# Optimization experiments

Measured on AMD Instinct MI355X. Metric: run time of the kernel, lower is better.

## Reference

```python
import jax, jax.numpy as jnp
import numpy as np
from functools import partial

THRESH = 0.5   # similarity_threshold
EPS = 1e-8     # F.cosine_similarity eps


def setup_inputs() -> dict:
    key = jax.random.key(0)
    # uniform positive vectors -> pairwise cosine ~0.75 > threshold, so merges actually occur
    embeddings = jax.random.uniform(key, (8192, 512), dtype=jnp.float32)
    return {"embeddings": embeddings}


@partial(jax.jit, static_argnums=())
def _greedy_match(embs):
    """One merge round. Returns (partner[i] or -1, consumed-as-j flag per i).
    Faithful to the original greedy: scan i in order; i picks argmax-sim j>i among
    not-yet-merged with sim >= threshold; both get marked merged."""
    n = embs.shape[0]
    norms = jnp.maximum(jnp.linalg.norm(embs, axis=-1), EPS)
    sim = (embs @ embs.T) / (norms[:, None] * norms[None, :])  # [n, n]
    idx = jnp.arange(n)

    def step(merged, xs):
        i, row = xs
        was_consumed = merged[i]
        valid = (~merged) & (idx > i)
        scores = jnp.where(valid, row, -jnp.inf)
        j = jnp.argmax(scores)
        ok = (~was_consumed) & (scores[j] >= THRESH)
        merged = merged.at[i].set(was_consumed | ok)
        merged = merged.at[j].set(merged[j] | ok)
        return merged, (jnp.where(ok, j, -1), was_consumed)

    _, (partners, consumed) = jax.lax.scan(step, jnp.zeros(n, bool), (idx, sim))
    return partners, consumed


def reference(embeddings):
    embs = embeddings
    # outer while-loop mirrors the module: iterate rounds until no merge or n<=1
    while embs.shape[0] > 1:
        partners, consumed = _greedy_match(embs)
        partners_np = np.asarray(partners)
        if not (partners_np >= 0).any():  # merge_occurred == False
            break
        safe = jnp.maximum(partners, 0)
        # fuse_embeddings: clamp(v1 + v2, max=1.0); non-leaders keep their row
        fused = jnp.where((partners >= 0)[:, None],
                          jnp.minimum(embs + embs[safe], 1.0), embs)
        survivors = np.where(~np.asarray(consumed))[0]  # rows not consumed as a j
        embs = fused[survivors]
    return embs
```

## Files before the change

kernel.cpp:

```cpp
#include <hip/hip_runtime.h>
#include <math.h>

#define D 512
#define THRESH 0.5f
#define NMAX 8192
#define TOPK 64

typedef short bhalf8 __attribute__((ext_vector_type(8)));
typedef float f32x4 __attribute__((ext_vector_type(4)));

__global__ void k_init(int* dn, int n) { *dn = n; }

__global__ void k_norms(const float* __restrict__ embs, float* __restrict__ norms,
                        const int* __restrict__ dn) {
    int n = *dn;
    int row = blockIdx.x;
    if (row >= n) return;
    int t = threadIdx.x;
    float4 v = ((const float4*)(embs + (size_t)row * D))[t];
    float s = v.x * v.x + v.y * v.y + v.z * v.z + v.w * v.w;
    #pragma unroll
    for (int o = 32; o > 0; o >>= 1) s += __shfl_down(s, o, 64);
    __shared__ float ls[2];
    if ((t & 63) == 0) ls[t >> 6] = s;
    __syncthreads();
    if (t == 0) norms[row] = fmaxf(sqrtf(ls[0] + ls[1]), 1e-8f);
}

__global__ void k_tobf16(const float* __restrict__ in, unsigned short* __restrict__ out,
                         const int* __restrict__ dn) {
    int n = *dn;
    size_t total = (size_t)n * D;
    size_t idx = ((size_t)blockIdx.x * 256 + threadIdx.x) * 8;
    if (idx >= total) return;
    float4 f0 = *(const float4*)(in + idx);
    float4 f1 = *(const float4*)(in + idx + 4);
    unsigned short r[8];
    float f[8] = {f0.x, f0.y, f0.z, f0.w, f1.x, f1.y, f1.z, f1.w};
    #pragma unroll
    for (int u = 0; u < 8; ++u) {
        unsigned int b = __float_as_uint(f[u]);
        r[u] = (unsigned short)((b + 0x7FFFu + ((b >> 16) & 1u)) >> 16);
    }
    uint4 packed;
    packed.x = (unsigned)r[0] | ((unsigned)r[1] << 16);
    packed.y = (unsigned)r[2] | ((unsigned)r[3] << 16);
    packed.z = (unsigned)r[4] | ((unsigned)r[5] << 16);
    packed.w = (unsigned)r[6] | ((unsigned)r[7] << 16);
    *(uint4*)(out + idx) = packed;
}

#define LDSTRIDE 72
__global__ void __launch_bounds__(256) k_mfma_sim(
    const unsigned short* __restrict__ H, const float* __restrict__ norms,
    float* __restrict__ sim, int tile_start, int TR, int simStride,
    const int* __restrict__ dn)
{
    int n = *dn;
    if (tile_start >= n) return;
    int row0 = tile_start + blockIdx.y * 128;
    int col0 = blockIdx.x * 128;
    if (row0 >= n || col0 >= n) return;
    if (col0 + 128 <= row0 + 1) return;

    __shared__ unsigned short As[128 * LDSTRIDE];
    __shared__ unsigned short Bs[128 * LDSTRIDE];
    int tid = threadIdx.x;
    int lane = tid & 63;
    int wave = tid >> 6;
    int wr = wave >> 1;
    int wc = wave & 1;
    int krow = lane & 15;
    int kgrp = (lane >> 4) * 8;

    f32x4 acc[4][4];
    #pragma unroll
    for (int m = 0; m < 4; ++m)
        #pragma unroll
        for (int t = 0; t < 4; ++t)
            acc[m][t] = (f32x4){0.f, 0.f, 0.f, 0.f};

    for (int k0 = 0; k0 < D; k0 += 64) {
        #pragma unroll
        for (int it = 0; it < 4; ++it) {
            int c  = tid + it * 256;
            int rr = c >> 3;
            int cc = c & 7;
            uint4 va = make_uint4(0, 0, 0, 0);
            int gra = row0 + rr;
            if (gra < n) va = *(const uint4*)(H + (size_t)gra * D + k0 + cc * 8);
            *(uint4*)&As[rr * LDSTRIDE + cc * 8] = va;
            uint4 vb = make_uint4(0, 0, 0, 0);
            int grb = col0 + rr;
            if (grb < n) vb = *(const uint4*)(H + (size_t)grb * D + k0 + cc * 8);
            *(uint4*)&Bs[rr * LDSTRIDE + cc * 8] = vb;
        }
        __syncthreads();
        #pragma unroll
        for (int kk = 0; kk < 64; kk += 32) {
            bhalf8 a[4], b[4];
            #pragma unroll
            for (int m = 0; m < 4; ++m)
                a[m] = *(const bhalf8*)&As[(wr * 64 + m * 16 + krow) * LDSTRIDE + kk + kgrp];
            #pragma unroll
            for (int t = 0; t < 4; ++t)
                b[t] = *(const bhalf8*)&Bs[(wc * 64 + t * 16 + krow) * LDSTRIDE + kk + kgrp];
            #pragma unroll
            for (int m = 0; m < 4; ++m)
                #pragma unroll
                for (int t = 0; t < 4; ++t)
                    acc[m][t] = __builtin_amdgcn_mfma_f32_16x16x32_bf16(a[m], b[t], acc[m][t], 0, 0, 0);
        }
        __syncthreads();
    }

    int fcol = lane & 15;
    int frow = (lane >> 4) * 4;
    #pragma unroll
    for (int m = 0; m < 4; ++m) {
        #pragma unroll
        for (int t = 0; t < 4; ++t) {
            #pragma unroll
            for (int v = 0; v < 4; ++v) {
                int gr = row0 + wr * 64 + m * 16 + frow + v;
                int gc = col0 + wc * 64 + t * 16 + fcol;
                if (gr < n && gc < n)
                    sim[(size_t)(gr - tile_start) * simStride + gc] =
                        acc[m][t][v] / (norms[gr] * norms[gc]);
            }
        }
    }
}

__global__ void __launch_bounds__(64) k_topk(
    const float* __restrict__ sim, int tile_start, int TR, int simStride,
    uint2* __restrict__ tkP, int* __restrict__ needFix,
    const int* __restrict__ dn)
{
    int n = *dn;
    int r = blockIdx.x;
    int i = tile_start + r;
    if (r >= TR || i >= n) return;
    int lane = threadIdx.x;
    const float* srow = sim + (size_t)r * simStride;

    float v[8]; int id[8];
    #pragma unroll
    for (int u = 0; u < 8; ++u) { v[u] = -INFINITY; id[u] = 0x7fffffff; }
    float ovV = -INFINITY; int ovI = 0x7fffffff;

    for (int j = i + 1 + lane; j < n; j += 64) {
        float x = srow[j];
        if (x > v[7] || (x == v[7] && j < id[7])) {
            if (v[7] > ovV || (v[7] == ovV && id[7] < ovI)) { ovV = v[7]; ovI = id[7]; }
            int p = 7;
            #pragma unroll
            for (int u = 6; u >= 0; --u) {
                bool mv = (x > v[u]) || (x == v[u] && j < id[u]);
                if (mv) { v[u + 1] = v[u]; id[u + 1] = id[u]; p = u; }
            }
            v[p] = x; id[p] = j;
        } else {
            if (x > ovV || (x == ovV && j < ovI)) { ovV = x; ovI = j; }
        }
    }

    int pos = 0;
    float myV = -INFINITY; int myI = 0x7fffffff;
    for (int k = 0; k < TOPK; ++k) {
        float hv = (pos < 8) ? v[pos] : -INFINITY;
        int   hi = (pos < 8) ? id[pos] : 0x7fffffff;
        float bv = hv; int bi = hi;
        #pragma unroll
        for (int o = 1; o < 64; o <<= 1) {
            float xv = __shfl_xor(bv, o, 64);
            int   xi = __shfl_xor(bi, o, 64);
            if (xv > bv || (xv == bv && xi < bi)) { bv = xv; bi = xi; }
        }
        if (pos < 8 && hv == bv && hi == bi) pos++;
        if (k == lane) { myV = bv; myI = bi; }
    }
    tkP[(size_t)i * TOPK + lane] = make_uint2(__float_as_uint(myV), (unsigned)myI);

    float v64 = __shfl(myV, 63, 64);
    int   i64 = __shfl(myI, 63, 64);
    float oV = ovV; int oI = ovI;
    #pragma unroll
    for (int o = 1; o < 64; o <<= 1) {
        float xv = __shfl_xor(oV, o, 64);
        int   xi = __shfl_xor(oI, o, 64);
        if (xv > oV || (xv == oV && xi < oI)) { oV = xv; oI = xi; }
    }
    int bad = (oV > v64) || (oV == v64 && oI < i64);
    if (lane == 0) needFix[i] = bad;
}

__global__ void __launch_bounds__(64) k_topkfix(
    const float* __restrict__ sim, int tile_start, int TR, int simStride,
    uint2* __restrict__ tkP, const int* __restrict__ needFix,
    const int* __restrict__ dn)
{
    int n = *dn;
    int r = blockIdx.x;
    int i = tile_start + r;
    if (r >= TR || i >= n) return;
    if (!needFix[i]) return;
    int lane = threadIdx.x;
    __shared__ float lv[64][TOPK];
    __shared__ int   li[64][TOPK];
    for (int u = 0; u < TOPK; ++u) { lv[lane][u] = -INFINITY; li[lane][u] = 0x7fffffff; }
    const float* srow = sim + (size_t)r * simStride;
    for (int j = i + 1 + lane; j < n; j += 64) {
        float x = srow[j];
        float wv = lv[lane][TOPK - 1]; int wi = li[lane][TOPK - 1];
        if (x > wv || (x == wv && j < wi)) {
            int p = TOPK - 1;
            for (int u = TOPK - 2; u >= 0; --u) {
                float uv = lv[lane][u]; int ui = li[lane][u];
                if (x > uv || (x == uv && j < ui)) { lv[lane][u + 1] = uv; li[lane][u + 1] = ui; p = u; }
                else break;
            }
            lv[lane][p] = x; li[lane][p] = j;
        }
    }
    int pos = 0;
    float myV = -INFINITY; int myI = 0x7fffffff;
    for (int k = 0; k < TOPK; ++k) {
        float hv = (pos < TOPK) ? lv[lane][pos] : -INFINITY;
        int   hi = (pos < TOPK) ? li[lane][pos] : 0x7fffffff;
        float bv = hv; int bi = hi;
        #pragma unroll
        for (int o = 1; o < 64; o <<= 1) {
            float xv = __shfl_xor(bv, o, 64);
            int   xi = __shfl_xor(bi, o, 64);
            if (xv > bv || (xv == bv && xi < bi)) { bv = xv; bi = xi; }
        }
        if (pos < TOPK && hv == bv && hi == bi) pos++;
        if (k == lane) { myV = bv; myI = bi; }
    }
    tkP[(size_t)i * TOPK + lane] = make_uint2(__float_as_uint(myV), (unsigned)myI);
}

__global__ void __launch_bounds__(64) k_scan4(
    const uint2* __restrict__ tkP,
    const float* __restrict__ E, const float* __restrict__ norms,
    int* __restrict__ partner, int* __restrict__ consumed,
    const int* __restrict__ dn)
{
    const int INF = 0x7fffffff;
    int n = *dn;
    int lane = threadIdx.x;

    for (int i = lane; i < n; i += 64) consumed[i] = 0;
    __threadfence();

    unsigned long long m0 = 0ull, m1 = 0ull;
    __shared__ unsigned int lm32[NMAX / 32];
    __shared__ int lsCnt;
    __shared__ int lsIdx[2048];

    int tLast = -1;

#define NEXT_UNMERGED(tt, outv) do {                                           \
    int base_ = lane << 7;                                                     \
    unsigned long long u0_ = ~m0, u1_ = ~m1;                                   \
    long long k_ = (long long)(tt) - base_ + 1;                                \
    if (k_ > 0) {                                                              \
        if (k_ >= 128) { u0_ = 0ull; u1_ = 0ull; }                             \
        else if (k_ >= 64) { u0_ = 0ull; if (k_ > 64) u1_ &= (~0ull) << (int)(k_ - 64); } \
        else u0_ &= (~0ull) << (int)k_;                                        \
    }                                                                          \
    int kn_ = n - base_;                                                       \
    if (kn_ <= 0) { u0_ = 0ull; u1_ = 0ull; }                                  \
    else if (kn_ < 64) { u0_ &= (~0ull) >> (64 - kn_); u1_ = 0ull; }           \
    else if (kn_ < 128) { u1_ = (kn_ == 64) ? 0ull : (u1_ & ((~0ull) >> (128 - kn_))); } \
    unsigned long long bal_ = __ballot((u0_ | u1_) != 0ull);                   \
    if (!bal_) { outv = INF; } else {                                          \
        int L_ = __builtin_ctzll(bal_);                                        \
        int cand_;                                                             \
        if (u0_ != 0ull) cand_ = (int)__builtin_ctzll(u0_);                    \
        else if (u1_ != 0ull) cand_ = 64 + (int)__builtin_ctzll(u1_);          \
        else cand_ = 0;                                                        \
        outv = (L_ << 7) + __shfl(cand_, L_, 64);                              \
    }                                                                          \
} while (0)

    int  selA[8]; uint2 cA[8];
    int  selB[8]; uint2 cB[8];

    #pragma unroll
    for (int k = 0; k < 8; ++k) {
        int nt; NEXT_UNMERGED(tLast, nt);
        selA[k] = nt;
        cA[k] = (nt < n) ? tkP[(size_t)nt * TOPK + lane]
                         : make_uint2(0xFF800000u, (unsigned)INF);
        tLast = nt;
    }

    int guard = NMAX + 64;
    while (selA[0] != INF && guard-- > 0) {
        #pragma unroll
        for (int k = 0; k < 8; ++k) {
            int nt; NEXT_UNMERGED(tLast, nt);
            selB[k] = nt;
            cB[k] = (nt < n) ? tkP[(size_t)nt * TOPK + lane]
                             : make_uint2(0xFF800000u, (unsigned)INF);
            tLast = nt;
        }
        #pragma unroll
        for (int k = 0; k < 8; ++k) {
            int r = selA[k];
            if (r == INF) continue;
            int ro = r >> 7;
            unsigned long long rw0 = __shfl(m0, ro, 64);
            unsigned long long rw1 = __shfl(m1, ro, 64);
            unsigned long long rw = (r & 64) ? rw1 : rw0;
            if ((rw >> (r & 63)) & 1ull) continue;

            int   ci = (int)cA[k].y;
            float cv = __uint_as_float(cA[k].x);
            int ow = (ci >> 7) & 63;
            unsigned long long w0 = __shfl(m0, ow, 64);
            unsigned long long w1 = __shfl(m1, ow, 64);
            unsigned long long w = (ci & 64) ? w1 : w0;
            bool valid = (ci < n) && !((w >> (ci & 63)) & 1ull);
            unsigned long long bal = __ballot(valid);
            int j = -1; float bv = -INFINITY;
            if (bal) {
                int L = __builtin_ctzll(bal);
                j  = (int)__shfl(ci, L, 64);
                bv = __shfl(cv, L, 64);
            } else {
                int nx; NEXT_UNMERGED(r, nx);
                if (nx != INF) {
                    ((unsigned long long*)lm32)[2 * lane + 0] = m0;
                    ((unsigned long long*)lm32)[2 * lane + 1] = m1;
                    float ni = norms[r];
                    float4 ei0 = *(const float4*)(E + (size_t)r * D + lane * 8);
                    float4 ei1 = *(const float4*)(E + (size_t)r * D + lane * 8 + 4);
                    float bbv = -INFINITY; int bbj = INF;
                    int w0i = (r + 1) >> 5, wN = (n + 31) >> 5;
                    for (int wb = w0i; wb < wN; wb += 64) {
                        if (lane == 0) lsCnt = 0;
                        int ww = wb + lane;
                        unsigned int um = 0u;
                        if (ww < wN) {
                            um = ~lm32[ww];
                            int jbase = ww << 5;
                            if (jbase <= r) {
                                int k2 = r - jbase + 1;
                                um &= (k2 >= 32) ? 0u : (0xffffffffu << k2);
                            }
                            int over = jbase + 32 - n;
                            if (over > 0) um &= (over >= 32) ? 0u : (0xffffffffu >> over);
                        }
                        while (um) {
                            int b = __builtin_ctz(um);
                            um &= um - 1;
                            lsIdx[atomicAdd(&lsCnt, 1)] = (ww << 5) + b;
                        }
                        int cnt = lsCnt;
                        for (int c = 0; c < cnt; ++c) {
                            int jj = lsIdx[c];
                            float4 a0 = *(const float4*)(E + (size_t)jj * D + lane * 8);
                            float4 a1 = *(const float4*)(E + (size_t)jj * D + lane * 8 + 4);
                            float s = ei0.x * a0.x + ei0.y * a0.y + ei0.z * a0.z + ei0.w * a0.w
                                    + ei1.x * a1.x + ei1.y * a1.y + ei1.z * a1.z + ei1.w * a1.w;
                            #pragma unroll
                            for (int o = 1; o < 64; o <<= 1) s += __shfl_xor(s, o, 64);
                            float sv = s / (ni * norms[jj]);
                            if (sv > bbv || (sv == bbv && jj < bbj)) { bbv = sv; bbj = jj; }
                        }
                    }
                    if (bbj != INF) { bv = bbv; j = bbj; }
                }
            }
            bool ok = (j >= 0) && (bv >= THRESH);
            if (ok) {
                if (lane == (r >> 7)) { if (r & 64) m1 |= 1ull << (r & 63); else m0 |= 1ull << (r & 63); }
                if (lane == (j >> 7)) { if (j & 64) m1 |= 1ull << (j & 63); else m0 |= 1ull << (j & 63); }
                if (lane == 0) { partner[r] = j; consumed[j] = 1; }
            } else {
                if (lane == 0) partner[r] = -1;
            }
        }
        #pragma unroll
        for (int k = 0; k < 8; ++k) { selA[k] = selB[k]; cA[k] = cB[k]; }
    }
#undef NEXT_UNMERGED
}

__global__ void __launch_bounds__(1024)
k_compact_plan(const int* __restrict__ consumed, int* __restrict__ srcIdx,
               int* __restrict__ dn) {
    int n = *dn;
    int t = threadIdx.x;
    __shared__ int lds[1024];
    __shared__ int base;
    if (t == 0) base = 0;
    __syncthreads();
    for (int c0 = 0; c0 < n; c0 += 1024) {
        int i = c0 + t;
        int f = (i < n) ? (consumed[i] ? 0 : 1) : 0;
        lds[t] = f;
        __syncthreads();
        for (int o = 1; o < 1024; o <<= 1) {
            int v = (t >= o) ? lds[t - o] : 0;
            __syncthreads();
            lds[t] += v;
            __syncthreads();
        }
        if (f) srcIdx[base + lds[t] - 1] = i;
        __syncthreads();
        if (t == 0) base += lds[1023];
        __syncthreads();
    }
    if (t == 0) *dn = base;
}

__global__ void k_fuse(const float* __restrict__ cur, float* __restrict__ nxt,
                       const int* __restrict__ srcIdx, const int* __restrict__ partner,
                       const int* __restrict__ dn) {
    int nn = *dn;
    int k = blockIdx.x;
    if (k >= nn) return;
    int t = threadIdx.x;
    int i = srcIdx[k];
    int p = partner[i];
    float4 v = ((const float4*)(cur + (size_t)i * D))[t];
    if (p >= 0) {
        float4 w = ((const float4*)(cur + (size_t)p * D))[t];
        v.x = fminf(v.x + w.x, 1.0f);
        v.y = fminf(v.y + w.y, 1.0f);
        v.z = fminf(v.z + w.z, 1.0f);
        v.w = fminf(v.w + w.w, 1.0f);
    }
    ((float4*)(nxt + (size_t)k * D))[t] = v;
}

__global__ void k_copyout(const float* __restrict__ src, float* __restrict__ dst, int nelem) {
    int i = blockIdx.x * 256 + threadIdx.x;
    if (i < nelem) dst[i] = src[i];
}

extern "C" void kernel_launch(void* const* d_in, const int* in_sizes, int n_in,
                              void* d_out, int out_size, void* d_ws, size_t ws_size,
                              hipStream_t stream) {
    const float* input = (const float*)d_in[0];
    const int N0 = in_sizes[0] / D;
    char* ws = (char*)d_ws;

    const size_t embA = (size_t)(N0 / 2) * D * sizeof(float);
    const size_t embB = (size_t)(N0 / 4) * D * sizeof(float);
    const size_t embH = (size_t)N0 * D * sizeof(unsigned short);
    float* bufA = (float*)ws;
    float* bufB = (float*)(ws + embA);
    unsigned short* curh = (unsigned short*)(ws + embA + embB);
    char* aux = ws + embA + embB + embH;
    float* norms   = (float*)(aux);
    int*   partner = (int*)(aux + 32 * 1024);
    int*   consumed= (int*)(aux + 64 * 1024);
    int*   srcIdx  = (int*)(aux + 96 * 1024);
    int*   dn      = (int*)(aux + 128 * 1024);
    int*   needFix = (int*)(aux + 160 * 1024);
    uint2* tkP     = (uint2*)(aux + 256 * 1024);
    float* simTile = (float*)(aux + 256 * 1024 + (size_t)NMAX * TOPK * 8);
    const size_t fixedBytes = embA + embB + embH + 256 * 1024 + (size_t)NMAX * TOPK * 8;

    int TR = NMAX;
    while (TR > 128 && fixedBytes + (size_t)TR * N0 * sizeof(float) > ws_size) TR >>= 1;

    const int ROUNDS = 16;
    k_init<<<1, 1, 0, stream>>>(dn, N0);
    for (int r = 0; r < ROUNDS; ++r) {
        const float* cur = (r == 0) ? input : ((r & 1) ? bufA : bufB);
        float* nxt = (r & 1) ? bufB : bufA;
        k_norms<<<N0, 128, 0, stream>>>(cur, norms, dn);
        k_tobf16<<<(N0 * D / 8 + 255) / 256, 256, 0, stream>>>(cur, curh, dn);
        int NT = N0 / TR;
        for (int t = 0; t < NT; ++t) {
            dim3 g(N0 / 128, TR / 128);
            k_mfma_sim<<<g, 256, 0, stream>>>(curh, norms, simTile, t * TR, TR, N0, dn);
            k_topk<<<TR, 64, 0, stream>>>(simTile, t * TR, TR, N0, tkP, needFix, dn);
            k_topkfix<<<TR, 64, 0, stream>>>(simTile, t * TR, TR, N0, tkP, needFix, dn);
        }
        k_scan4<<<1, 64, 0, stream>>>(tkP, cur, norms, partner, consumed, dn);
        k_compact_plan<<<1, 1024, 0, stream>>>(consumed, srcIdx, dn);
        k_fuse<<<N0, 128, 0, stream>>>(cur, nxt, srcIdx, partner, dn);
    }
    float* fin = bufB;
    k_copyout<<<(out_size + 255) / 256, 256, 0, stream>>>(fin, (float*)d_out, out_size);
}
```

Before: 15.59 ms.

## Batch greedy scan into 8-row groups with ballot-precomputed validity and fused compaction

Rewrites the serial greedy matching scan so it gathers eight unmerged rows at once and computes their candidate-validity ballots together. It then resolves the rows in order, checking only for collisions with partners chosen earlier in the same batch, which aims to cut the per-row serial latency of the single-wavefront scan. The consumed-flag compaction kernel is folded into the scan as a wave-level prefix sum over a consumed bitmask. The norms and bf16 conversion kernels are merged into one prep kernel. The batched collision logic is more complex and risks subtle ordering bugs.

```diff
diff --git a/kernel.cpp b/kernel.cpp
--- a/kernel.cpp
+++ b/kernel.cpp
@@ -5,49 +5,38 @@
 #define THRESH 0.5f
 #define NMAX 8192
 #define TOPK 64
+#define INFI 0x7fffffff
 
 typedef short bhalf8 __attribute__((ext_vector_type(8)));
 typedef float f32x4 __attribute__((ext_vector_type(4)));
 
 __global__ void k_init(int* dn, int n) { *dn = n; }
 
-__global__ void k_norms(const float* __restrict__ embs, float* __restrict__ norms,
-                        const int* __restrict__ dn) {
+__global__ void k_prep(const float* __restrict__ E, float* __restrict__ norms,
+                       unsigned short* __restrict__ H, const int* __restrict__ dn) {
     int n = *dn;
     int row = blockIdx.x;
     if (row >= n) return;
     int t = threadIdx.x;
-    float4 v = ((const float4*)(embs + (size_t)row * D))[t];
+    float4 v = ((const float4*)(E + (size_t)row * D))[t];
     float s = v.x * v.x + v.y * v.y + v.z * v.z + v.w * v.w;
     #pragma unroll
     for (int o = 32; o > 0; o >>= 1) s += __shfl_down(s, o, 64);
     __shared__ float ls[2];
     if ((t & 63) == 0) ls[t >> 6] = s;
+    float f[4] = {v.x, v.y, v.z, v.w};
+    unsigned short r[4];
+    #pragma unroll
+    for (int u = 0; u < 4; ++u) {
+        unsigned int b = __float_as_uint(f[u]);
+        r[u] = (unsigned short)((b + 0x7FFFu + ((b >> 16) & 1u)) >> 16);
+    }
+    uint2 packed;
+    packed.x = (unsigned)r[0] | ((unsigned)r[1] << 16);
+    packed.y = (unsigned)r[2] | ((unsigned)r[3] << 16);
+    *(uint2*)(H + (size_t)row * D + t * 4) = packed;
     __syncthreads();
     if (t == 0) norms[row] = fmaxf(sqrtf(ls[0] + ls[1]), 1e-8f);
-}
-
-__global__ void k_tobf16(const float* __restrict__ in, unsigned short* __restrict__ out,
-                         const int* __restrict__ dn) {
-    int n = *dn;
-    size_t total = (size_t)n * D;
-    size_t idx = ((size_t)blockIdx.x * 256 + threadIdx.x) * 8;
-    if (idx >= total) return;
-    float4 f0 = *(const float4*)(in + idx);
-    float4 f1 = *(const float4*)(in + idx + 4);
-    unsigned short r[8];
-    float f[8] = {f0.x, f0.y, f0.z, f0.w, f1.x, f1.y, f1.z, f1.w};
-    #pragma unroll
-    for (int u = 0; u < 8; ++u) {
-        unsigned int b = __float_as_uint(f[u]);
-        r[u] = (unsigned short)((b + 0x7FFFu + ((b >> 16) & 1u)) >> 16);
-    }
-    uint4 packed;
-    packed.x = (unsigned)r[0] | ((unsigned)r[1] << 16);
-    packed.y = (unsigned)r[2] | ((unsigned)r[3] << 16);
-    packed.z = (unsigned)r[4] | ((unsigned)r[5] << 16);
-    packed.w = (unsigned)r[6] | ((unsigned)r[7] << 16);
-    *(uint4*)(out + idx) = packed;
 }
 
 #define LDSTRIDE 72
@@ -146,8 +135,8 @@
 
     float v[8]; int id[8];
     #pragma unroll
-    for (int u = 0; u < 8; ++u) { v[u] = -INFINITY; id[u] = 0x7fffffff; }
-    float ovV = -INFINITY; int ovI = 0x7fffffff;
+    for (int u = 0; u < 8; ++u) { v[u] = -INFINITY; id[u] = INFI; }
+    float ovV = -INFINITY; int ovI = INFI;
 
     for (int j = i + 1 + lane; j < n; j += 64) {
         float x = srow[j];
@@ -166,10 +155,10 @@
     }
 
     int pos = 0;
-    float myV = -INFINITY; int myI = 0x7fffffff;
+    float myV = -INFINITY; int myI = INFI;
     for (int k = 0; k < TOPK; ++k) {
         float hv = (pos < 8) ? v[pos] : -INFINITY;
-        int   hi = (pos < 8) ? id[pos] : 0x7fffffff;
+        int   hi = (pos < 8) ? id[pos] : INFI;
         float bv = hv; int bi = hi;
         #pragma unroll
         for (int o = 1; o < 64; o <<= 1) {
@@ -208,7 +197,7 @@
     int lane = threadIdx.x;
     __shared__ float lv[64][TOPK];
     __shared__ int   li[64][TOPK];
-    for (int u = 0; u < TOPK; ++u) { lv[lane][u] = -INFINITY; li[lane][u] = 0x7fffffff; }
+    for (int u = 0; u < TOPK; ++u) { lv[lane][u] = -INFINITY; li[lane][u] = INFI; }
     const float* srow = sim + (size_t)r * simStride;
     for (int j = i + 1 + lane; j < n; j += 64) {
         float x = srow[j];
@@ -224,10 +213,10 @@
         }
     }
     int pos = 0;
-    float myV = -INFINITY; int myI = 0x7fffffff;
+    float myV = -INFINITY; int myI = INFI;
     for (int k = 0; k < TOPK; ++k) {
         float hv = (pos < TOPK) ? lv[lane][pos] : -INFINITY;
-        int   hi = (pos < TOPK) ? li[lane][pos] : 0x7fffffff;
+        int   hi = (pos < TOPK) ? li[lane][pos] : INFI;
         float bv = hv; int bi = hi;
         #pragma unroll
         for (int o = 1; o < 64; o <<= 1) {
@@ -241,181 +230,209 @@
     tkP[(size_t)i * TOPK + lane] = make_uint2(__float_as_uint(myV), (unsigned)myI);
 }
 
-__global__ void __launch_bounds__(64) k_scan4(
+__device__ __attribute__((noinline)) void exact_fallback(
+    int r, int n, int lane, const float* __restrict__ E,
+    const float* __restrict__ norms, const unsigned long long* lm64,
+    float& obv, int& obj)
+{
+    float ni = norms[r];
+    float4 e0 = *(const float4*)(E + (size_t)r * D + lane * 8);
+    float4 e1 = *(const float4*)(E + (size_t)r * D + lane * 8 + 4);
+    float bbv = -INFINITY; int bbj = INFI;
+    int w0 = (r + 1) >> 6, wN = (n + 63) >> 6;
+    for (int ww = w0; ww < wN; ++ww) {
+        unsigned long long um = ~lm64[ww];
+        if (ww == (r >> 6)) um &= (~0ull) << ((r & 63) + 1);
+        int over = (ww << 6) + 64 - n;
+        if (over > 0) um &= (over >= 64) ? 0ull : ((~0ull) >> over);
+        while (um) {
+            int b = __builtin_ctzll(um);
+            um &= um - 1;
+            int jj = (ww << 6) + b;
+            float4 a0 = *(const float4*)(E + (size_t)jj * D + lane * 8);
+            float4 a1 = *(const float4*)(E + (size_t)jj * D + lane * 8 + 4);
+            float s = e0.x * a0.x + e0.y * a0.y + e0.z * a0.z + e0.w * a0.w
+                    + e1.x * a1.x + e1.y * a1.y + e1.z * a1.z + e1.w * a1.w;
+            #pragma unroll
+            for (int o = 1; o < 64; o <<= 1) s += __shfl_xor(s, o, 64);
+            float sv = s / (ni * norms[jj]);
+            if (sv > bbv || (sv == bbv && jj < bbj)) { bbv = sv; bbj = jj; }
+        }
+    }
+    obv = bbv; obj = bbj;
+}
+
+__global__ void __launch_bounds__(64) k_scan5(
     const uint2* __restrict__ tkP,
     const float* __restrict__ E, const float* __restrict__ norms,
-    int* __restrict__ partner, int* __restrict__ consumed,
-    const int* __restrict__ dn)
+    int* __restrict__ partner, int* __restrict__ srcIdx,
+    int* __restrict__ dn)
 {
-    const int INF = 0x7fffffff;
     int n = *dn;
     int lane = threadIdx.x;
 
-    for (int i = lane; i < n; i += 64) consumed[i] = 0;
-    __threadfence();
-
     unsigned long long m0 = 0ull, m1 = 0ull;
-    __shared__ unsigned int lm32[NMAX / 32];
-    __shared__ int lsCnt;
-    __shared__ int lsIdx[2048];
-
-    int tLast = -1;
-
-#define NEXT_UNMERGED(tt, outv) do {                                           \
-    int base_ = lane << 7;                                                     \
-    unsigned long long u0_ = ~m0, u1_ = ~m1;                                   \
-    long long k_ = (long long)(tt) - base_ + 1;                                \
-    if (k_ > 0) {                                                              \
-        if (k_ >= 128) { u0_ = 0ull; u1_ = 0ull; }                             \
+    unsigned long long cm0 = 0ull, cm1 = 0ull;
+    __shared__ unsigned long long lm64[NMAX / 64];
+
+    int nextStart = 0;
+    const uint2 SENT = make_uint2(0xFF800000u, (unsigned)INFI);
+
+#define DECL8(P, C) int P##0=INFI,P##1=INFI,P##2=INFI,P##3=INFI,P##4=INFI,P##5=INFI,P##6=INFI,P##7=INFI; \
+                    uint2 C##0=SENT,C##1=SENT,C##2=SENT,C##3=SENT,C##4=SENT,C##5=SENT,C##6=SENT,C##7=SENT;
+
+#define BUILD(P, C) do {                                                        \
+    P##0=INFI;P##1=INFI;P##2=INFI;P##3=INFI;P##4=INFI;P##5=INFI;P##6=INFI;P##7=INFI; \
+    int base_ = lane << 7;                                                      \
+    unsigned long long u0_ = ~m0, u1_ = ~m1;                                    \
+    long long k_ = (long long)nextStart - base_;                                \
+    if (k_ > 0) {                                                               \
+        if (k_ >= 128) { u0_ = 0ull; u1_ = 0ull; }                              \
         else if (k_ >= 64) { u0_ = 0ull; if (k_ > 64) u1_ &= (~0ull) << (int)(k_ - 64); } \
-        else u0_ &= (~0ull) << (int)k_;                                        \
-    }                                                                          \
-    int kn_ = n - base_;                                                       \
-    if (kn_ <= 0) { u0_ = 0ull; u1_ = 0ull; }                                  \
-    else if (kn_ < 64) { u0_ &= (~0ull) >> (64 - kn_); u1_ = 0ull; }           \
+        else u0_ &= (~0ull) << (int)k_;                                         \
+    }                                                                           \
+    int kn_ = n - base_;                                                        \
+    if (kn_ <= 0) { u0_ = 0ull; u1_ = 0ull; }                                   \
+    else if (kn_ < 64) { u0_ &= (~0ull) >> (64 - kn_); u1_ = 0ull; }            \
     else if (kn_ < 128) { u1_ = (kn_ == 64) ? 0ull : (u1_ & ((~0ull) >> (128 - kn_))); } \
-    unsigned long long bal_ = __ballot((u0_ | u1_) != 0ull);                   \
-    if (!bal_) { outv = INF; } else {                                          \
-        int L_ = __builtin_ctzll(bal_);                                        \
-        int cand_;                                                             \
-        if (u0_ != 0ull) cand_ = (int)__builtin_ctzll(u0_);                    \
-        else if (u1_ != 0ull) cand_ = 64 + (int)__builtin_ctzll(u1_);          \
-        else cand_ = 0;                                                        \
-        outv = (L_ << 7) + __shfl(cand_, L_, 64);                              \
-    }                                                                          \
+    unsigned long long balv_ = __ballot((u0_ | u1_) != 0ull);                   \
+    int got_ = 0, lastSel_ = -1;                                                \
+    while (got_ < 8 && balv_) {                                                 \
+        int L_ = __builtin_ctzll(balv_); balv_ &= balv_ - 1;                    \
+        unsigned long long w0_ = __shfl(u0_, L_, 64);                           \
+        unsigned long long w1_ = __shfl(u1_, L_, 64);                           \
+        int bs_ = L_ << 7;                                                      \
+        while (w0_ && got_ < 8) { int b_ = __builtin_ctzll(w0_); w0_ &= w0_-1;  \
+            int v_ = bs_ + b_; lastSel_ = v_; SETSEL(P, got_, v_); got_++; }    \
+        while (w1_ && got_ < 8) { int b_ = __builtin_ctzll(w1_); w1_ &= w1_-1;  \
+            int v_ = bs_ + 64 + b_; lastSel_ = v_; SETSEL(P, got_, v_); got_++; } \
+    }                                                                           \
+    nextStart = (got_ > 0) ? (lastSel_ + 1) : n;                                \
+    C##0 = (P##0 < n) ? tkP[(size_t)P##0 * TOPK + lane] : SENT;                 \
+    C##1 = (P##1 < n) ? tkP[(size_t)P##1 * TOPK + lane] : SENT;                 \
+    C##2 = (P##2 < n) ? tkP[(size_t)P##2 * TOPK + lane] : SENT;                 \
+    C##3 = (P##3 < n) ? tkP[(size_t)P##3 * TOPK + lane] : SENT;                 \
+    C##4 = (P##4 < n) ? tkP[(size_t)P##4 * TOPK + lane] : SENT;                 \
+    C##5 = (P##5 < n) ? tkP[(size_t)P##5 * TOPK + lane] : SENT;                 \
+    C##6 = (P##6 < n) ? tkP[(size_t)P##6 * TOPK + lane] : SENT;                 \
+    C##7 = (P##7 < n) ? tkP[(size_t)P##7 * TOPK + lane] : SENT;                 \
 } while (0)
 
-    int  selA[8]; uint2 cA[8];
-    int  selB[8]; uint2 cB[8];
-
-    #pragma unroll
-    for (int k = 0; k < 8; ++k) {
-        int nt; NEXT_UNMERGED(tLast, nt);
-        selA[k] = nt;
-        cA[k] = (nt < n) ? tkP[(size_t)nt * TOPK + lane]
-                         : make_uint2(0xFF800000u, (unsigned)INF);
-        tLast = nt;
-    }
-
-    int guard = NMAX + 64;
-    while (selA[0] != INF && guard-- > 0) {
-        #pragma unroll
-        for (int k = 0; k < 8; ++k) {
-            int nt; NEXT_UNMERGED(tLast, nt);
-            selB[k] = nt;
-            cB[k] = (nt < n) ? tkP[(size_t)nt * TOPK + lane]
-                             : make_uint2(0xFF800000u, (unsigned)INF);
-            tLast = nt;
-        }
-        #pragma unroll
-        for (int k = 0; k < 8; ++k) {
-            int r = selA[k];
-            if (r == INF) continue;
-            int ro = r >> 7;
-            unsigned long long rw0 = __shfl(m0, ro, 64);
-            unsigned long long rw1 = __shfl(m1, ro, 64);
-            unsigned long long rw = (r & 64) ? rw1 : rw0;
-            if ((rw >> (r & 63)) & 1ull) continue;
-
-            int   ci = (int)cA[k].y;
-            float cv = __uint_as_float(cA[k].x);
-            int ow = (ci >> 7) & 63;
-            unsigned long long w0 = __shfl(m0, ow, 64);
-            unsigned long long w1 = __shfl(m1, ow, 64);
-            unsigned long long w = (ci & 64) ? w1 : w0;
-            bool valid = (ci < n) && !((w >> (ci & 63)) & 1ull);
-            unsigned long long bal = __ballot(valid);
-            int j = -1; float bv = -INFINITY;
-            if (bal) {
-                int L = __builtin_ctzll(bal);
-                j  = (int)__shfl(ci, L, 64);
-                bv = __shfl(cv, L, 64);
-            } else {
-                int nx; NEXT_UNMERGED(r, nx);
-                if (nx != INF) {
-                    ((unsigned long long*)lm32)[2 * lane + 0] = m0;
-                    ((unsigned long long*)lm32)[2 * lane + 1] = m1;
-                    float ni = norms[r];
-                    float4 ei0 = *(const float4*)(E + (size_t)r * D + lane * 8);
-                    float4 ei1 = *(const float4*)(E + (size_t)r * D + lane * 8 + 4);
-                    float bbv = -INFINITY; int bbj = INF;
-                    int w0i = (r + 1) >> 5, wN = (n + 31) >> 5;
-                    for (int wb = w0i; wb < wN; wb += 64) {
-                        if (lane == 0) lsCnt = 0;
-                        int ww = wb + lane;
-                        unsigned int um = 0u;
-                        if (ww < wN) {
-                            um = ~lm32[ww];
-                            int jbase = ww << 5;
-                            if (jbase <= r) {
-                                int k2 = r - jbase + 1;
-                                um &= (k2 >= 32) ? 0u : (0xffffffffu << k2);
-                            }
-                            int over = jbase + 32 - n;
-                            if (over > 0) um &= (over >= 32) ? 0u : (0xffffffffu >> over);
-                        }
-                        while (um) {
-                            int b = __builtin_ctz(um);
-                            um &= um - 1;
-                            lsIdx[atomicAdd(&lsCnt, 1)] = (ww << 5) + b;
-                        }
-                        int cnt = lsCnt;
-                        for (int c = 0; c < cnt; ++c) {
-                            int jj = lsIdx[c];
-                            float4 a0 = *(const float4*)(E + (size_t)jj * D + lane * 8);
-                            float4 a1 = *(const float4*)(E + (size_t)jj * D + lane * 8 + 4);
-                            float s = ei0.x * a0.x + ei0.y * a0.y + ei0.z * a0.z + ei0.w * a0.w
-                                    + ei1.x * a1.x + ei1.y * a1.y + ei1.z * a1.z + ei1.w * a1.w;
-                            #pragma unroll
-                            for (int o = 1; o < 64; o <<= 1) s += __shfl_xor(s, o, 64);
-                            float sv = s / (ni * norms[jj]);
-                            if (sv > bbv || (sv == bbv && jj < bbj)) { bbv = sv; bbj = jj; }
-                        }
-                    }
-                    if (bbj != INF) { bv = bbv; j = bbj; }
-                }
-            }
-            bool ok = (j >= 0) && (bv >= THRESH);
-            if (ok) {
-                if (lane == (r >> 7)) { if (r & 64) m1 |= 1ull << (r & 63); else m0 |= 1ull << (r & 63); }
-                if (lane == (j >> 7)) { if (j & 64) m1 |= 1ull << (j & 63); else m0 |= 1ull << (j & 63); }
-                if (lane == 0) { partner[r] = j; consumed[j] = 1; }
-            } else {
-                if (lane == 0) partner[r] = -1;
-            }
-        }
-        #pragma unroll
-        for (int k = 0; k < 8; ++k) { selA[k] = selB[k]; cA[k] = cB[k]; }
-    }
-#undef NEXT_UNMERGED
-}
-
-__global__ void __launch_bounds__(1024)
-k_compact_plan(const int* __restrict__ consumed, int* __restrict__ srcIdx,
-               int* __restrict__ dn) {
-    int n = *dn;
-    int t = threadIdx.x;
-    __shared__ int lds[1024];
-    __shared__ int base;
-    if (t == 0) base = 0;
-    __syncthreads();
-    for (int c0 = 0; c0 < n; c0 += 1024) {
-        int i = c0 + t;
-        int f = (i < n) ? (consumed[i] ? 0 : 1) : 0;
-        lds[t] = f;
-        __syncthreads();
-        for (int o = 1; o < 1024; o <<= 1) {
-            int v = (t >= o) ? lds[t - o] : 0;
-            __syncthreads();
-            lds[t] += v;
-            __syncthreads();
-        }
-        if (f) srcIdx[base + lds[t] - 1] = i;
-        __syncthreads();
-        if (t == 0) base += lds[1023];
-        __syncthreads();
-    }
-    if (t == 0) *dn = base;
+#define SETSEL(P, g, v) {                                                       \
+    if ((g)==0) P##0=(v); else if ((g)==1) P##1=(v); else if ((g)==2) P##2=(v); \
+    else if ((g)==3) P##3=(v); else if ((g)==4) P##4=(v); else if ((g)==5) P##5=(v); \
+    else if ((g)==6) P##6=(v); else P##7=(v); }
+
+#define SETBIT(v) { if (lane == (((v) >> 7) & 63)) {                            \
+    if ((v) & 64) m1 |= 1ull << ((v) & 63); else m0 |= 1ull << ((v) & 63); } }
+#define SETCM(v)  { if (lane == (((v) >> 7) & 63)) {                            \
+    if ((v) & 64) cm1 |= 1ull << ((v) & 63); else cm0 |= 1ull << ((v) & 63); } }
+
+#define PH1(P, C, k) unsigned long long vb##k = 0ull; bool rm##k = false;       \
+    if (P##k != INFI) {                                                         \
+        int r_ = P##k;                                                          \
+        unsigned long long rw_ = __shfl((r_ & 64) ? m1 : m0, (r_ >> 7) & 63, 64); \
+        rm##k = (rw_ >> (r_ & 63)) & 1ull;                                      \
+        int ci_ = (int)C##k.y;                                                  \
+        int ow_ = (ci_ >> 7) & 63;                                              \
+        unsigned long long w0_ = __shfl(m0, ow_, 64);                           \
+        unsigned long long w1_ = __shfl(m1, ow_, 64);                           \
+        unsigned long long ws_ = (ci_ & 64) ? w1_ : w0_;                        \
+        bool val_ = (ci_ < n) && !((ws_ >> (ci_ & 63)) & 1ull);                 \
+        vb##k = __ballot(val_);                                                 \
+    }
+
+#define JCOLL(x) ((x)==jj0||(x)==jj1||(x)==jj2||(x)==jj3||(x)==jj4||(x)==jj5||(x)==jj6||(x)==jj7)
+
+#define RES(P, C, k) if (P##k != INFI && !rm##k && !JCOLL(P##k)) {              \
+    int r_ = P##k;                                                              \
+    unsigned long long w_ = vb##k;                                              \
+    int j_ = -1; float v_ = -INFINITY;                                          \
+    for (;;) {                                                                  \
+        if (!w_) break;                                                         \
+        int L_ = __builtin_ctzll(w_);                                           \
+        int jc_ = __shfl((int)C##k.y, L_, 64);                                  \
+        if (JCOLL(jc_)) { w_ &= w_ - 1; continue; }                             \
+        j_ = jc_;                                                               \
+        v_ = __uint_as_float((unsigned)__shfl((int)C##k.x, L_, 64));            \
+        break;                                                                  \
+    }                                                                           \
+    if (j_ < 0) {                                                               \
+                           \
+        int base_ = lane << 7;                                                  \
+        unsigned long long u0_ = ~m0, u1_ = ~m1;                                \
+        long long kk_ = (long long)(r_ + 1) - base_;                            \
+        if (kk_ > 0) {                                                          \
+            if (kk_ >= 128) { u0_ = 0ull; u1_ = 0ull; }                         \
+            else if (kk_ >= 64) { u0_ = 0ull; if (kk_ > 64) u1_ &= (~0ull) << (int)(kk_ - 64); } \
+            else u0_ &= (~0ull) << (int)kk_;                                    \
+        }                                                                       \
+        int kn_ = n - base_;                                                    \
+        if (kn_ <= 0) { u0_ = 0ull; u1_ = 0ull; }                               \
+        else if (kn_ < 64) { u0_ &= (~0ull) >> (64 - kn_); u1_ = 0ull; }        \
+        else if (kn_ < 128) { u1_ = (kn_ == 64) ? 0ull : (u1_ & ((~0ull) >> (128 - kn_))); } \
+        if (__ballot((u0_ | u1_) != 0ull)) {                                    \
+            lm64[2 * lane]     = m0;                                            \
+            lm64[2 * lane + 1] = m1;                                            \
+            exact_fallback(r_, n, lane, E, norms, lm64, v_, j_);                \
+            if (j_ == INFI) j_ = -1;                                            \
+        }                                                                       \
+    }                                                                           \
+    bool ok_ = (j_ >= 0) && (v_ >= THRESH);                                     \
+    if (ok_) {                                                                  \
+        SETBIT(r_); SETBIT(j_); SETCM(j_);                                      \
+        jj##k = j_;                                                             \
+        if (lane == 0) partner[r_] = j_;                                        \
+    } else {                                                                    \
+        if (lane == 0) partner[r_] = -1;                                        \
+    }                                                                           \
+}
+
+    DECL8(ra, ca)
+    DECL8(rb, cb)
+
+    BUILD(ra, ca);
+    int guard = NMAX + 8;
+    while (ra0 != INFI && guard-- > 0) {
+        BUILD(rb, cb);
+        {
+            PH1(ra, ca, 0) PH1(ra, ca, 1) PH1(ra, ca, 2) PH1(ra, ca, 3)
+            PH1(ra, ca, 4) PH1(ra, ca, 5) PH1(ra, ca, 6) PH1(ra, ca, 7)
+            int jj0=-1,jj1=-1,jj2=-1,jj3=-1,jj4=-1,jj5=-1,jj6=-1,jj7=-1;
+            RES(ra, ca, 0) RES(ra, ca, 1) RES(ra, ca, 2) RES(ra, ca, 3)
+            RES(ra, ca, 4) RES(ra, ca, 5) RES(ra, ca, 6) RES(ra, ca, 7)
+        }
+        ra0=rb0; ra1=rb1; ra2=rb2; ra3=rb3; ra4=rb4; ra5=rb5; ra6=rb6; ra7=rb7;
+        ca0=cb0; ca1=cb1; ca2=cb2; ca3=cb3; ca4=cb4; ca5=cb5; ca6=cb6; ca7=cb7;
+    }
+
+    {
+        int base = lane << 7;
+        unsigned long long s0 = ~cm0, s1 = ~cm1;
+        int kn = n - base;
+        if (kn <= 0) { s0 = 0ull; s1 = 0ull; }
+        else if (kn < 64) { s0 &= (~0ull) >> (64 - kn); s1 = 0ull; }
+        else if (kn < 128) { s1 = (kn == 64) ? 0ull : (s1 & ((~0ull) >> (128 - kn))); }
+        int cnt = __builtin_popcountll(s0) + __builtin_popcountll(s1);
+        int inc = cnt;
+        #pragma unroll
+        for (int o = 1; o < 64; o <<= 1) {
+            int t = __shfl_up(inc, o, 64);
+            if (lane >= o) inc += t;
+        }
+        int p = inc - cnt;
+        while (s0) { int b = __builtin_ctzll(s0); s0 &= s0 - 1; srcIdx[p++] = base + b; }
+        while (s1) { int b = __builtin_ctzll(s1); s1 &= s1 - 1; srcIdx[p++] = base + 64 + b; }
+        if (lane == 63) *dn = inc;
+    }
+#undef DECL8
+#undef BUILD
+#undef SETSEL
+#undef SETBIT
+#undef SETCM
+#undef PH1
+#undef JCOLL
+#undef RES
 }
 
 __global__ void k_fuse(const float* __restrict__ cur, float* __restrict__ nxt,
@@ -459,7 +476,6 @@
     char* aux = ws + embA + embB + embH;
     float* norms   = (float*)(aux);
     int*   partner = (int*)(aux + 32 * 1024);
-    int*   consumed= (int*)(aux + 64 * 1024);
     int*   srcIdx  = (int*)(aux + 96 * 1024);
     int*   dn      = (int*)(aux + 128 * 1024);
     int*   needFix = (int*)(aux + 160 * 1024);
@@ -475,8 +491,7 @@
     for (int r = 0; r < ROUNDS; ++r) {
         const float* cur = (r == 0) ? input : ((r & 1) ? bufA : bufB);
         float* nxt = (r & 1) ? bufB : bufA;
-        k_norms<<<N0, 128, 0, stream>>>(cur, norms, dn);
-        k_tobf16<<<(N0 * D / 8 + 255) / 256, 256, 0, stream>>>(cur, curh, dn);
+        k_prep<<<N0, 128, 0, stream>>>(cur, norms, curh, dn);
         int NT = N0 / TR;
         for (int t = 0; t < NT; ++t) {
             dim3 g(N0 / 128, TR / 128);
@@ -484,8 +499,7 @@
             k_topk<<<TR, 64, 0, stream>>>(simTile, t * TR, TR, N0, tkP, needFix, dn);
             k_topkfix<<<TR, 64, 0, stream>>>(simTile, t * TR, TR, N0, tkP, needFix, dn);
         }
-        k_scan4<<<1, 64, 0, stream>>>(tkP, cur, norms, partner, consumed, dn);
-        k_compact_plan<<<1, 1024, 0, stream>>>(consumed, srcIdx, dn);
+        k_scan5<<<1, 64, 0, stream>>>(tkP, cur, norms, partner, srcIdx, dn);
         k_fuse<<<N0, 128, 0, stream>>>(cur, nxt, srcIdx, partner, dn);
     }
     float* fin = bufB;
```

Measured after the change: 17.29 ms. +10.9%, slower.
